# Optimization experiments

Measured on AMD Instinct MI355X. Metric: run time of the kernel, lower is better.

The kernel has to match this reference:

```python
import jax, jax.numpy as jnp
import numpy as np

# dims
B, T, NM, F = 2, 32512, 80, 128          # batch, samples, n_mels, frames
R, S, NC = 64, 128, 256                   # residual, skip, num_class channels
HOP, UK, KC = 256, 512, 2                 # hopsize, upsample kernel, causal kernel
MD, NCB = 10, 3                           # dilations per cycle (2^0..2^9), cycles
NB = MD * NCB                             # 30 residual blocks


def conv1d(x, w, b, dilation=1, pad=(0, 0), lhs_dilation=1):
    # x: [B,C,L], w: [O,I,K] (OIH), b: [O]
    y = jax.lax.conv_general_dilated(
        x, w, window_strides=(1,), padding=(pad,),
        lhs_dilation=(lhs_dilation,), rhs_dilation=(dilation,),
        dimension_numbers=('NCH', 'OIH', 'NCH'))
    return y + b[None, :, None]


def setup_inputs() -> dict:
    key = jax.random.key(0)
    ks = jax.random.split(key, 16)
    s = 0.05
    nrm = lambda k, shape: jax.random.normal(k, shape, dtype=jnp.float32) * s
    return {
        'x': jax.random.normal(ks[0], (B, T), dtype=jnp.float32),
        'mels': jax.random.normal(ks[1], (B, NM, F), dtype=jnp.float32),
        'input_w': nrm(ks[2], (R, 1, 1)), 'input_b': jnp.zeros((R,), jnp.float32),
        # mel upsampler (ConvTranspose1d), kernel stored in forward-conv OIH layout
        'mel_w': nrm(ks[3], (NM, NM, UK)), 'mel_b': jnp.zeros((NM,), jnp.float32),
        # 30 gated residual blocks, params stacked on leading axis
        'blk_dil_w': nrm(ks[4], (NB, 2 * R, R, KC)), 'blk_dil_b': jnp.zeros((NB, 2 * R), jnp.float32),
        'blk_cond_w': nrm(ks[5], (NB, 2 * R, NM, 1)), 'blk_cond_b': jnp.zeros((NB, 2 * R), jnp.float32),
        'blk_skip_w': nrm(ks[6], (NB, S, R, 1)), 'blk_skip_b': jnp.zeros((NB, S), jnp.float32),
        'blk_res_w': nrm(ks[7], (NB, R, R, 1)), 'blk_res_b': jnp.zeros((NB, R), jnp.float32),
        'post1_w': nrm(ks[8], (NC, S, 1)), 'post1_b': jnp.zeros((NC,), jnp.float32),
        'post2_w': nrm(ks[9], (NC, NC, 1)), 'post2_b': jnp.zeros((NC,), jnp.float32),
    }


def reference(x, mels, input_w, input_b, mel_w, mel_b,
              blk_dil_w, blk_dil_b, blk_cond_w, blk_cond_b,
              blk_skip_w, blk_skip_b, blk_res_w, blk_res_b,
              post1_w, post1_b, post2_w, post2_b):
    # ConvTranspose1d(stride=HOP, padding=UK//2) == lhs-dilated conv with pad UK-1-UK//2
    pt = UK - 1 - UK // 2
    cond = conv1d(mels, mel_w, mel_b, pad=(pt, pt), lhs_dilation=HOP)  # [B,NM,(F-1)*HOP]
    L = min(T, cond.shape[-1])
    cond = cond[..., :L]
    res = conv1d(x[:, None, :L], input_w, input_b)  # [B,R,L]
    skip = jnp.zeros((B, S, L), res.dtype)
    for i in range(NB):
        d = 2 ** (i % MD)
        z = (conv1d(res, blk_dil_w[i], blk_dil_b[i], dilation=d, pad=((KC - 1) * d, 0))
             + conv1d(cond, blk_cond_w[i], blk_cond_b[i]))  # [B,2R,L]
        f, g = jnp.split(z, 2, axis=1)
        h = jnp.tanh(f) * jax.nn.sigmoid(g)                 # gated activation
        skip = skip + conv1d(h, blk_skip_w[i], blk_skip_b[i])
        res = res + conv1d(h, blk_res_w[i], blk_res_b[i])
    y = conv1d(jax.nn.relu(skip), post1_w, post1_b)
    y = conv1d(jax.nn.relu(y), post2_w, post2_b)            # [B,NC,L]
    return y
```

## Files before the change

### kernel.cpp

```cpp
#include <hip/hip_runtime.h>
#include <math.h>

#define T_LEN 32512
#define NTILES 508
#define BATCH 2
#define NMEL 80
#define FRAMES 128
#define NBLK 30
#define NPAIRS 15
#define PAD 768
#define TP (T_LEN + PAD)

typedef short bfrag __attribute__((ext_vector_type(8)));
typedef float facc __attribute__((ext_vector_type(4)));
typedef ushort us4v __attribute__((ext_vector_type(4)));
typedef ushort us8v __attribute__((ext_vector_type(8)));

#define MFMA16(a, b, c) __builtin_amdgcn_mfma_f32_16x16x32_bf16((a), (b), (c), 0, 0, 0)

#define RESH_OFF   0u
#define CONDB_OFF  17039360u
#define WA_OFF     29818880u
#define WSF_OFF    31539200u
#define WRF_OFF    32030720u
#define WP1_OFF    32276480u
#define WP2_OFF    32342016u
#define ZB_OFF     32473088u
#define SBS_OFF    32488448u
#define SKIPG_OFF  32488960u
#define CONDA_OFF  SKIPG_OFF
#define HB_OFF     65781248u
#define SLOT_BYTES 8323072ull
#define SLOT_ELEMS 4161536ull
#define Y1R_OFF    82427392u
#undef Y1R_OFF
#define Y1R_OFF    165658112u

static __device__ __forceinline__ ushort f2bf(float f) {
  union { float f; unsigned int u; } v;
  v.f = f;
  unsigned int r = (v.u + 0x7FFFu + ((v.u >> 16) & 1u)) >> 16;
  return (ushort)r;
}
static __device__ __forceinline__ float bf2f(ushort h) {
  union { unsigned int u; float f; } v;
  v.u = ((unsigned int)h) << 16;
  return v.f;
}
static __device__ __forceinline__ float sigmoidf_(float x) {
  return 1.f / (1.f + __expf(-x));
}
static __device__ __forceinline__ float tanhf_(float x) {
  return 2.f / (1.f + __expf(-2.f * x)) - 1.f;
}
static __device__ __forceinline__ bfrag ldfrag(const ushort* p) {
  return *reinterpret_cast<const bfrag*>(p);
}
static __device__ __forceinline__ void gload_lds16(const void* g, void* l) {
  __builtin_amdgcn_global_load_lds(
      (const __attribute__((address_space(1))) unsigned int*)g,
      (__attribute__((address_space(3))) unsigned int*)l, 16, 0, 0);
}

__global__ __launch_bounds__(256) void prep_kernel(
    const float* __restrict__ dil_w, const float* __restrict__ cond_w,
    const float* __restrict__ skip_w, const float* __restrict__ res_w,
    const float* __restrict__ p1_w, const float* __restrict__ p2_w,
    const float* __restrict__ mel_w, const float* __restrict__ dil_b,
    const float* __restrict__ cond_b, const float* __restrict__ skip_b,
    ushort* __restrict__ wa, ushort* __restrict__ wsf, ushort* __restrict__ wrf,
    ushort* __restrict__ wp1, ushort* __restrict__ wp2,
    ushort* __restrict__ condA, float* __restrict__ zb,
    float* __restrict__ sbs) {
  int tid = blockIdx.x * blockDim.x + threadIdx.x;
  int stride = gridDim.x * blockDim.x;
  for (int idx = tid; idx < NBLK * 56 * 512; idx += stride) {
    int j = idx & 7, lane = (idx >> 3) & 63;
    int f = (idx >> 9) % 56, layer = idx / (56 * 512);
    int mt = f / 7, kt = f % 7;
    int m = 16 * mt + (lane & 15);
    int k = 32 * kt + 8 * (lane >> 4) + j;
    float v;
    if (k < 64)       v = dil_w[(((size_t)layer * 128 + m) * 64 + k) * 2 + 0];
    else if (k < 128) v = dil_w[(((size_t)layer * 128 + m) * 64 + (k - 64)) * 2 + 1];
    else if (k < 208) v = cond_w[((size_t)layer * 128 + m) * 80 + (k - 128)];
    else              v = 0.f;
    wa[idx] = f2bf(v);
  }
  for (int idx = tid; idx < NBLK * 16 * 512; idx += stride) {
    int j = idx & 7, lane = (idx >> 3) & 63;
    int f = (idx >> 9) & 15, layer = idx / (16 * 512);
    int mt = f >> 1, kt = f & 1;
    int m = 16 * mt + (lane & 15);
    int k = 32 * kt + 8 * (lane >> 4) + j;
    wsf[idx] = f2bf(skip_w[((size_t)layer * 128 + m) * 64 + k]);
  }
  for (int idx = tid; idx < NBLK * 8 * 512; idx += stride) {
    int j = idx & 7, lane = (idx >> 3) & 63;
    int f = (idx >> 9) & 7, layer = idx / (8 * 512);
    int mt = f >> 1, kt = f & 1;
    int m = 16 * mt + (lane & 15);
    int k = 32 * kt + 8 * (lane >> 4) + j;
    wrf[idx] = f2bf(res_w[((size_t)layer * 64 + m) * 64 + k]);
  }
  for (int idx = tid; idx < 64 * 512; idx += stride) {
    int j = idx & 7, lane = (idx >> 3) & 63;
    int f = idx >> 9;
    int mt = f >> 2, kt = f & 3;
    int m = 16 * mt + (lane & 15);
    int k = 32 * kt + 8 * (lane >> 4) + j;
    wp1[idx] = f2bf(p1_w[(size_t)m * 128 + k]);
  }
  for (int idx = tid; idx < 128 * 512; idx += stride) {
    int j = idx & 7, lane = (idx >> 3) & 63;
    int f = idx >> 9;
    int mt = f >> 3, kt = f & 7;
    int m = 16 * mt + (lane & 15);
    int k = 32 * kt + 8 * (lane >> 4) + j;
    wp2[idx] = f2bf(p2_w[(size_t)m * 256 + k]);
  }
  for (int idx = tid; idx < 25 * 512 * 256; idx += stride) {
    int q = idx & 511;
    int f = (idx >> 9) % 25;
    int u = idx / (25 * 512);
    int j = q & 7, lane = q >> 3;
    int mt = f / 5, kt = f % 5;
    int m = 16 * mt + (lane & 15);
    int k = 32 * kt + 8 * (lane >> 4) + j;
    int ci = (k < 80) ? k : k - 80;
    int kk = (k < 80) ? (255 - u) : (511 - u);
    condA[idx] = f2bf(mel_w[((size_t)m * 80 + ci) * 512 + kk]);
  }
  for (int idx = tid; idx < NBLK * 128; idx += stride)
    zb[idx] = dil_b[idx] + cond_b[idx];
  for (int idx = tid; idx < 128; idx += stride) {
    float s = 0.f;
    for (int i2 = 0; i2 < NBLK; ++i2) s += skip_b[i2 * 128 + idx];
    sbs[idx] = s;
  }
}

#define BSTR 168
__global__ __launch_bounds__(256) void cond_mfma(
    const float* __restrict__ mels, const ushort* __restrict__ condA,
    const float* __restrict__ mel_b, ushort* __restrict__ condb) {
  __shared__ ushort BT[128 * BSTR];
  const int tid = threadIdx.x;
  const int lane = tid & 63;
  const int w = tid >> 6;
  const int b = blockIdx.y;
  const int half = blockIdx.z;
  const int u = blockIdx.x * 4 + w;
  const int q4 = 4 * (lane >> 4);
  const int l15 = lane & 15;
  const float* melb = mels + (size_t)b * NMEL * FRAMES;
  for (int idx = tid; idx < 160 * 128; idx += 256) {
    int M = idx & 127;
    int k = idx >> 7;
    int ci = (k < 80) ? k : k - 80;
    int Mp = M + ((k < 80) ? 0 : 1);
    float v = (Mp < 128) ? melb[(size_t)ci * FRAMES + Mp] : 0.f;
    BT[M * BSTR + k] = f2bf(v);
  }
  __syncthreads();
  facc acc[5][4];
  #pragma unroll
  for (int mt = 0; mt < 5; ++mt) {
    #pragma unroll
    for (int nt = 0; nt < 4; ++nt) {
      #pragma unroll
      for (int r = 0; r < 4; ++r) acc[mt][nt][r] = mel_b[16 * mt + q4 + r];
    }
  }
  const ushort* cA = condA + (size_t)u * 25 * 512 + lane * 8;
  const int bofs = l15 * BSTR + 8 * (lane >> 4);
  #pragma unroll
  for (int kt = 0; kt < 5; ++kt) {
    bfrag a[5];
    #pragma unroll
    for (int mt = 0; mt < 5; ++mt) a[mt] = ldfrag(cA + (mt * 5 + kt) * 512);
    #pragma unroll
    for (int nt = 0; nt < 4; ++nt) {
      bfrag bb = ldfrag(&BT[(half * 64 + nt * 16) * BSTR + bofs + kt * 32]);
      #pragma unroll
      for (int mt = 0; mt < 5; ++mt) acc[mt][nt] = MFMA16(a[mt], bb, acc[mt][nt]);
    }
  }
  ushort* cbp = condb + (size_t)b * TP * 96;
  #pragma unroll
  for (int mt = 0; mt < 5; ++mt) {
    #pragma unroll
    for (int nt = 0; nt < 4; ++nt) {
      const int M = half * 64 + nt * 16 + l15;
      if (M < 127) {
        us4v p;
        #pragma unroll
        for (int r = 0; r < 4; ++r) p[r] = f2bf(acc[mt][nt][r]);
        const int t = M * 256 + u;
        *reinterpret_cast<us4v*>(&cbp[(size_t)(t + PAD) * 96 + 16 * mt + q4]) = p;
      }
    }
  }
}

__global__ __launch_bounds__(256) void init_res_kernel(
    const float* __restrict__ x, const float* __restrict__ iw,
    const float* __restrict__ ib, ushort* __restrict__ resh0) {
  int idx = blockIdx.x * blockDim.x + threadIdx.x;
  if (idx >= BATCH * T_LEN * 64) return;
  int c = idx & 63;
  int t = (idx >> 6) % T_LEN;
  int b = idx / (64 * T_LEN);
  float v = x[(size_t)b * T_LEN + t] * iw[c] + ib[c];
  resh0[(size_t)b * TP * 64 + (size_t)(t + PAD) * 64 + c] = f2bf(v);
}

template <int DEFER>
__global__ __launch_bounds__(256, 4) void wn_pair_kernel(
    const ushort* __restrict__ resh_in, ushort* __restrict__ resh_out,
    const ushort* __restrict__ condb, const ushort* __restrict__ wa,
    const ushort* __restrict__ wsf, const ushort* __restrict__ wrf,
    const float* __restrict__ zb, const float* __restrict__ res_b,
    const float* __restrict__ skip_b, float* __restrict__ skipg,
    ushort* __restrict__ hb0, ushort* __restrict__ hb1, int i0, int d0,
    int writeRes) {
  __shared__ ushort HT[64 * 72];
  __shared__ ushort RTs[64 * 72];
  __shared__ ushort RTh[64 * 72];
  const int i1 = i0 + 1;
  const int d1 = 2 * d0;
  const int tid = threadIdx.x;
  const int lane = tid & 63;
  const int w = tid >> 6;
  const int l15 = lane & 15;
  const int q4 = 4 * (lane >> 4);
  const int colq = 8 * (lane >> 4);
  const int orig = blockIdx.x;
  const int xcd = orig & 7;
  const int loc = orig >> 3;
  const int tile = (xcd < 4 ? xcd * 64 : 256 + (xcd - 4) * 63) + loc;
  const int t0 = tile * 64;
  const int t0s = t0 - d1;
  const int b = blockIdx.y;

  const ushort* rhi = resh_in + (size_t)b * TP * 64;
  ushort* rho = resh_out + (size_t)b * TP * 64;
  const ushort* cbp = condb + (size_t)b * TP * 96;
  const int bofs_h = l15 * 72 + colq;

  facc rs_s[4], rs_h[4], sk[8];
  facc accF[4], accG[4];
  if constexpr (!DEFER) {
    #pragma unroll
    for (int j = 0; j < 8; ++j) {
      const int ch = 32 * w + 16 * (j >> 2) + q4;
      facc s0 = *(const facc*)(skip_b + i0 * 128 + ch);
      facc s1 = *(const facc*)(skip_b + i1 * 128 + ch);
      sk[j] = s0 + s1;
    }
  }

#define ZG_INITB(LAYER)                                                       \
  _Pragma("unroll")                                                           \
  for (int nt = 0; nt < 4; ++nt) {                                            \
    accF[nt] = *(const facc*)(zb + (LAYER) * 128 + 16 * w + q4);              \
    accG[nt] = *(const facc*)(zb + (LAYER) * 128 + 64 + 16 * w + q4);         \
  }

#define ZG_GLOBAL(LAYER, TB)                                                  \
  {                                                                           \
    ZG_INITB(LAYER)                                                           \
    const ushort* wal = wa + (size_t)(LAYER) * 56 * 512 + lane * 8;           \
    const ushort* bp0[4];                                                     \
    const ushort* bp1[4];                                                     \
    const ushort* bpc[4];                                                     \
    _Pragma("unroll")                                                         \
    for (int nt = 0; nt < 4; ++nt) {                                          \
      const int tg = (TB) + nt * 16 + l15;                                    \
      bp0[nt] = rhi + (size_t)(tg - d0 + PAD) * 64 + colq;                    \
      bp1[nt] = rhi + (size_t)(tg + PAD) * 64 + colq;                         \
      bpc[nt] = cbp + (size_t)(tg + PAD) * 96 + colq;                         \
    }                                                                         \
    _Pragma("unroll")                                                         \
    for (int kt = 0; kt < 7; ++kt) {                                          \
      bfrag aF = ldfrag(wal + (w * 7 + kt) * 512);                            \
      bfrag aG = ldfrag(wal + ((w + 4) * 7 + kt) * 512);                      \
      _Pragma("unroll")                                                       \
      for (int nt = 0; nt < 4; ++nt) {                                        \
        bfrag bb = (kt < 2)   ? ldfrag(bp0[nt] + kt * 32)                     \
                   : (kt < 4) ? ldfrag(bp1[nt] + (kt - 2) * 32)               \
                              : ldfrag(bpc[nt] + (kt - 4) * 32);              \
        accF[nt] = MFMA16(aF, bb, accF[nt]);                                  \
        accG[nt] = MFMA16(aG, bb, accG[nt]);                                  \
      }                                                                       \
    }                                                                         \
  }

#define ZG_LDS(LAYER)                                                        \
  {                                                                           \
    ZG_INITB(LAYER)                                                           \
    const ushort* wal = wa + (size_t)(LAYER) * 56 * 512 + lane * 8;           \
    const ushort* bpc[4];                                                     \
    _Pragma("unroll")                                                         \
    for (int nt = 0; nt < 4; ++nt)                                            \
      bpc[nt] = cbp + (size_t)(t0 + nt * 16 + l15 + PAD) * 96 + colq;         \
    _Pragma("unroll")                                                         \
    for (int kt = 0; kt < 7; ++kt) {                                          \
      bfrag aF = ldfrag(wal + (w * 7 + kt) * 512);                            \
      bfrag aG = ldfrag(wal + ((w + 4) * 7 + kt) * 512);                      \
      _Pragma("unroll")                                                       \
      for (int nt = 0; nt < 4; ++nt) {                                        \
        bfrag bb = (kt < 2)                                                   \
            ? ldfrag(&RTs[(nt * 16 + l15) * 72 + kt * 32 + colq])             \
            : (kt < 4)                                                        \
                ? ldfrag(&RTh[(nt * 16 + l15) * 72 + (kt - 2) * 32 + colq])   \
                : ldfrag(bpc[nt] + (kt - 4) * 32);                            \
        accF[nt] = MFMA16(aF, bb, accF[nt]);                                  \
        accG[nt] = MFMA16(aG, bb, accG[nt]);                                  \
      }                                                                       \
    }                                                                         \
  }

#define GATE(HBPTR, DOHB)                                                     \
  {                                                                           \
    _Pragma("unroll")                                                         \
    for (int nt = 0; nt < 4; ++nt) {                                          \
      us4v p;                                                                 \
      _Pragma("unroll")                                                       \
      for (int r = 0; r < 4; ++r)                                             \
        p[r] = f2bf(tanhf_(accF[nt][r]) * sigmoidf_(accG[nt][r]));            \
      *reinterpret_cast<us4v*>(&HT[(nt * 16 + l15) * 72 + 16 * w + q4]) = p;  \
      if (DOHB)                                                               \
        *reinterpret_cast<us4v*>((HBPTR) + (size_t)b * T_LEN * 64 +           \
                                 (size_t)(t0 + nt * 16 + l15) * 64 +          \
                                 16 * w + q4) = p;                            \
    }                                                                         \
  }

#define RES_GEMM(LAYER, RS)                                                   \
  {                                                                           \
    const ushort* wrl = wrf + (size_t)(LAYER) * 8 * 512 + lane * 8;           \
    _Pragma("unroll")                                                         \
    for (int kt = 0; kt < 2; ++kt) {                                          \
      bfrag ar = ldfrag(wrl + (w * 2 + kt) * 512);                            \
      _Pragma("unroll")                                                       \
      for (int nt = 0; nt < 4; ++nt) {                                        \
        bfrag bb = ldfrag(&HT[nt * 16 * 72 + bofs_h + kt * 32]);              \
        RS[nt] = MFMA16(ar, bb, RS[nt]);                                      \
      }                                                                       \
    }                                                                         \
  }

#define SKIP_GEMM(LAYER)                                                      \
  {                                                                           \
    const ushort* wsl = wsf + (size_t)(LAYER) * 16 * 512 + lane * 8;          \
    _Pragma("unroll")                                                         \
    for (int kt = 0; kt < 2; ++kt) {                                          \
      bfrag a0 = ldfrag(wsl + ((2 * w) * 2 + kt) * 512);                      \
      bfrag a1 = ldfrag(wsl + ((2 * w + 1) * 2 + kt) * 512);                  \
      _Pragma("unroll")                                                       \
      for (int nt = 0; nt < 4; ++nt) {                                        \
        bfrag bb = ldfrag(&HT[nt * 16 * 72 + bofs_h + kt * 32]);              \
        sk[nt] = MFMA16(a0, bb, sk[nt]);                                      \
        sk[4 + nt] = MFMA16(a1, bb, sk[4 + nt]);                              \
      }                                                                       \
    }                                                                         \
  }

  ZG_GLOBAL(i0, t0s);
  GATE(hb0, 0);
  __syncthreads();
  #pragma unroll
  for (int nt = 0; nt < 4; ++nt) {
    const int tg = t0s + nt * 16 + l15;
    us4v hv = *(const us4v*)(rhi + (size_t)(tg + PAD) * 64 + 16 * w + q4);
    facc rbv = *(const facc*)(res_b + i0 * 64 + 16 * w + q4);
    #pragma unroll
    for (int r = 0; r < 4; ++r) rs_s[nt][r] = bf2f(hv[r]) + rbv[r];
  }
  RES_GEMM(i0, rs_s);
  #pragma unroll
  for (int nt = 0; nt < 4; ++nt) {
    const bool ok = (t0s + nt * 16 + l15) >= 0;
    us4v p;
    #pragma unroll
    for (int r = 0; r < 4; ++r) p[r] = ok ? f2bf(rs_s[nt][r]) : (ushort)0;
    *reinterpret_cast<us4v*>(&RTs[(nt * 16 + l15) * 72 + 16 * w + q4]) = p;
  }
  __syncthreads();
  ZG_GLOBAL(i0, t0);
  GATE(hb0, DEFER);
  __syncthreads();
  #pragma unroll
  for (int nt = 0; nt < 4; ++nt) {
    const int tg = t0 + nt * 16 + l15;
    us4v hv = *(const us4v*)(rhi + (size_t)(tg + PAD) * 64 + 16 * w + q4);
    facc rbv = *(const facc*)(res_b + i0 * 64 + 16 * w + q4);
    #pragma unroll
    for (int r = 0; r < 4; ++r) rs_h[nt][r] = bf2f(hv[r]) + rbv[r];
  }
  if constexpr (!DEFER) { SKIP_GEMM(i0); }
  RES_GEMM(i0, rs_h);
  #pragma unroll
  for (int nt = 0; nt < 4; ++nt) {
    us4v p;
    #pragma unroll
    for (int r = 0; r < 4; ++r) p[r] = f2bf(rs_h[nt][r]);
    *reinterpret_cast<us4v*>(&RTh[(nt * 16 + l15) * 72 + 16 * w + q4]) = p;
  }
  __syncthreads();
  ZG_LDS(i1);
  GATE(hb1, DEFER);
  __syncthreads();
  #pragma unroll
  for (int nt = 0; nt < 4; ++nt) {
    facc rbv = *(const facc*)(res_b + i1 * 64 + 16 * w + q4);
    rs_s[nt] = rs_h[nt] + rbv;
  }
  if constexpr (!DEFER) { SKIP_GEMM(i1); }
  RES_GEMM(i1, rs_s);
  if (writeRes) {
    #pragma unroll
    for (int nt = 0; nt < 4; ++nt) {
      const int tg = t0 + nt * 16 + l15;
      us4v p;
      #pragma unroll
      for (int r = 0; r < 4; ++r) p[r] = f2bf(rs_s[nt][r]);
      *reinterpret_cast<us4v*>(rho + (size_t)(tg + PAD) * 64 + 16 * w + q4) = p;
    }
  }
  if constexpr (!DEFER) {
    float* sg = skipg + (size_t)b * T_LEN * 128;
    #pragma unroll
    for (int nt = 0; nt < 4; ++nt) {
      const int tg = t0 + nt * 16 + l15;
      facc* p0 = (facc*)(sg + (size_t)tg * 128 + 32 * w + q4);
      facc* p1 = (facc*)(sg + (size_t)tg * 128 + 32 * w + 16 + q4);
      *p0 = *p0 + sk[nt];
      *p1 = *p1 + sk[4 + nt];
    }
  }
#undef ZG_INITB
#undef ZG_GLOBAL
#undef ZG_LDS
#undef GATE
#undef RES_GEMM
#undef SKIP_GEMM
}

template <int FIRST, int FUSE>
__global__ __launch_bounds__(256) void skip_accum(
    const ushort* __restrict__ hb, const ushort* __restrict__ wsf,
    float* __restrict__ skipg, const float* __restrict__ sbs,
    const ushort* __restrict__ wp1, const float* __restrict__ p1b,
    ushort* __restrict__ y1r, int base, int nl) {
  __shared__ ushort HL[12 * 2048];
  const int tid = threadIdx.x;
  const int lane = tid & 63;
  const int w = tid >> 6;
  const int l15 = lane & 15;
  const int q4 = 4 * (lane >> 4);
  const int colq = 8 * (lane >> 4);
  const int t0 = blockIdx.x * 32;
  const int b = blockIdx.y;

  {
    const int D = tid * 16;
    const int Dsw = D ^ (((D >> 7) & 7) << 4);
    const char* srcb =
        (const char*)(hb + (size_t)b * T_LEN * 64 + (size_t)t0 * 64);
    char* ldsb = (char*)HL + (tid >> 6) * 1024;
    for (int l = 0; l < nl; ++l)
      gload_lds16(srcb + (size_t)l * SLOT_BYTES + Dsw, ldsb + l * 4096);
  }

  float* sg = skipg + (size_t)b * T_LEN * 128;
  facc a0[2], a1[2];
  if constexpr (FIRST) {
    #pragma unroll
    for (int nt = 0; nt < 2; ++nt) {
      #pragma unroll
      for (int r = 0; r < 4; ++r) { a0[nt][r] = 0.f; a1[nt][r] = 0.f; }
    }
  } else {
    #pragma unroll
    for (int nt = 0; nt < 2; ++nt) {
      const int tg = t0 + nt * 16 + l15;
      a0[nt] = *(const facc*)(sg + (size_t)tg * 128 + 32 * w + q4);
      a1[nt] = *(const facc*)(sg + (size_t)tg * 128 + 32 * w + 16 + q4);
    }
  }
  __syncthreads();

  for (int l = 0; l < nl; ++l) {
    const ushort* wsl = wsf + (size_t)(base + l) * 16 * 512 + lane * 8;
    #pragma unroll
    for (int kt = 0; kt < 2; ++kt) {
      bfrag f0 = ldfrag(wsl + ((2 * w) * 2 + kt) * 512);
      bfrag f1 = ldfrag(wsl + ((2 * w + 1) * 2 + kt) * 512);
      #pragma unroll
      for (int nt = 0; nt < 2; ++nt) {
        const int t = nt * 16 + l15;
        int byteoff = t * 128 + kt * 64 + colq * 2;
        byteoff ^= ((t & 7) << 4);
        bfrag bb = ldfrag((const ushort*)((const char*)HL + l * 4096 + byteoff));
        a0[nt] = MFMA16(f0, bb, a0[nt]);
        a1[nt] = MFMA16(f1, bb, a1[nt]);
      }
    }
  }

  if constexpr (!FUSE) {
    #pragma unroll
    for (int nt = 0; nt < 2; ++nt) {
      const int tg = t0 + nt * 16 + l15;
      *(facc*)(sg + (size_t)tg * 128 + 32 * w + q4) = a0[nt];
      *(facc*)(sg + (size_t)tg * 128 + 32 * w + 16 + q4) = a1[nt];
    }
  } else {
    __syncthreads();
    ushort* ST = HL;
    #pragma unroll
    for (int nt = 0; nt < 2; ++nt) {
      us4v p0, p1;
      #pragma unroll
      for (int r = 0; r < 4; ++r) {
        p0[r] = f2bf(fmaxf(a0[nt][r] + sbs[32 * w + q4 + r], 0.f));
        p1[r] = f2bf(fmaxf(a1[nt][r] + sbs[32 * w + 16 + q4 + r], 0.f));
      }
      const int row = nt * 16 + l15;
      *reinterpret_cast<us4v*>(&ST[row * 136 + 32 * w + q4]) = p0;
      *reinterpret_cast<us4v*>(&ST[row * 136 + 32 * w + 16 + q4]) = p1;
    }
    __syncthreads();
    facc acc2[4][2];
    #pragma unroll
    for (int mi = 0; mi < 4; ++mi) {
      #pragma unroll
      for (int nt = 0; nt < 2; ++nt) {
        #pragma unroll
        for (int r = 0; r < 4; ++r)
          acc2[mi][nt][r] = p1b[16 * (4 * w + mi) + q4 + r];
      }
    }
    const int lo = lane * 8;
    #pragma unroll
    for (int kt = 0; kt < 4; ++kt) {
      bfrag am[4];
      #pragma unroll
      for (int mi = 0; mi < 4; ++mi)
        am[mi] = ldfrag(wp1 + ((4 * w + mi) * 4 + kt) * 512 + lo);
      #pragma unroll
      for (int nt = 0; nt < 2; ++nt) {
        bfrag bb = ldfrag(&ST[(nt * 16 + l15) * 136 + kt * 32 + colq]);
        #pragma unroll
        for (int mi = 0; mi < 4; ++mi)
          acc2[mi][nt] = MFMA16(am[mi], bb, acc2[mi][nt]);
      }
    }
    ushort* yb = y1r + (size_t)b * 256 * T_LEN;
    #pragma unroll
    for (int mi = 0; mi < 4; ++mi) {
      #pragma unroll
      for (int nt = 0; nt < 2; ++nt) {
        const int tt = t0 + nt * 16 + l15;
        #pragma unroll
        for (int r = 0; r < 4; ++r)
          yb[(size_t)(16 * (4 * w + mi) + q4 + r) * T_LEN + tt] =
              f2bf(fmaxf(acc2[mi][nt][r], 0.f));
      }
    }
  }
}

#define FSSTR 136
__global__ __launch_bounds__(256) void post1_mfma(
    const float* __restrict__ skipg, const float* __restrict__ sbs,
    const ushort* __restrict__ wp1, const float* __restrict__ p1b,
    ushort* __restrict__ y1r) {
  __shared__ ushort ST[64 * FSSTR];
  const int tid = threadIdx.x;
  const int lane = tid & 63;
  const int w = tid >> 6;
  const int t0 = blockIdx.x * 64;
  const int b = blockIdx.y;
  {
    const int t = tid & 63;
    const int kc = tid >> 6;
    const float* sp =
        skipg + (size_t)b * T_LEN * 128 + (size_t)(t0 + t) * 128 + kc * 32;
    #pragma unroll
    for (int j = 0; j < 8; ++j) {
      facc v = *(const facc*)(sp + j * 4);
      us4v o;
      #pragma unroll
      for (int r = 0; r < 4; ++r) {
        float s = sbs ? sbs[kc * 32 + j * 4 + r] : 0.f;
        o[r] = f2bf(fmaxf(v[r] + s, 0.f));
      }
      *reinterpret_cast<us4v*>(&ST[t * FSSTR + kc * 32 + j * 4]) = o;
    }
  }
  __syncthreads();
  const int q4 = 4 * (lane >> 4);
  facc acc[4][4];
  #pragma unroll
  for (int mi = 0; mi < 4; ++mi) {
    #pragma unroll
    for (int nt = 0; nt < 4; ++nt) {
      #pragma unroll
      for (int r = 0; r < 4; ++r)
        acc[mi][nt][r] = p1b[16 * (4 * w + mi) + q4 + r];
    }
  }
  const int lo = lane * 8;
  const int bofs = (lane & 15) * FSSTR + 8 * (lane >> 4);
  #pragma unroll
  for (int kt = 0; kt < 4; ++kt) {
    bfrag a[4];
    #pragma unroll
    for (int mi = 0; mi < 4; ++mi)
      a[mi] = ldfrag(wp1 + ((4 * w + mi) * 4 + kt) * 512 + lo);
    #pragma unroll
    for (int nt = 0; nt < 4; ++nt) {
      bfrag bb = ldfrag(&ST[nt * 16 * FSSTR + bofs + kt * 32]);
      #pragma unroll
      for (int mi = 0; mi < 4; ++mi) acc[mi][nt] = MFMA16(a[mi], bb, acc[mi][nt]);
    }
  }
  ushort* yb = y1r + (size_t)b * 256 * T_LEN;
  #pragma unroll
  for (int mi = 0; mi < 4; ++mi) {
    #pragma unroll
    for (int nt = 0; nt < 4; ++nt) {
      const int tt = t0 + nt * 16 + (lane & 15);
      #pragma unroll
      for (int r = 0; r < 4; ++r)
        yb[(size_t)(16 * (4 * w + mi) + q4 + r) * T_LEN + tt] =
            f2bf(fmaxf(acc[mi][nt][r], 0.f));
    }
  }
}

#define YSTR 264
__global__ __launch_bounds__(256) void post2_mfma(
    const ushort* __restrict__ y1r, const ushort* __restrict__ wp2,
    const float* __restrict__ p2b, float* __restrict__ out) {
  __shared__ ushort YT[64 * YSTR];
  const int tid = threadIdx.x;
  const int lane = tid & 63;
  const int w = tid >> 6;
  const int t0 = blockIdx.x * 64;
  const int b = blockIdx.y;
  const ushort* yb = y1r + (size_t)b * 256 * T_LEN;
  const int t = t0 + lane;
  for (int kc = 0; kc < 8; ++kc) {
    int k0 = w * 64 + kc * 8;
    us8v v;
    #pragma unroll
    for (int j = 0; j < 8; ++j) v[j] = yb[(size_t)(k0 + j) * T_LEN + t];
    *reinterpret_cast<us8v*>(&YT[lane * YSTR + k0]) = v;
  }
  __syncthreads();
  const int q4 = 4 * (lane >> 4);
  facc acc[4][4];
  #pragma unroll
  for (int mi = 0; mi < 4; ++mi) {
    #pragma unroll
    for (int nt = 0; nt < 4; ++nt) {
      #pragma unroll
      for (int r = 0; r < 4; ++r)
        acc[mi][nt][r] = p2b[16 * (4 * w + mi) + q4 + r];
    }
  }
  const int lo = lane * 8;
  const int bofs = (lane & 15) * YSTR + 8 * (lane >> 4);
  #pragma unroll
  for (int kt = 0; kt < 8; ++kt) {
    bfrag a[4];
    #pragma unroll
    for (int mi = 0; mi < 4; ++mi)
      a[mi] = ldfrag(wp2 + ((4 * w + mi) * 8 + kt) * 512 + lo);
    #pragma unroll
    for (int nt = 0; nt < 4; ++nt) {
      bfrag bb = ldfrag(&YT[nt * 16 * YSTR + bofs + kt * 32]);
      #pragma unroll
      for (int mi = 0; mi < 4; ++mi) acc[mi][nt] = MFMA16(a[mi], bb, acc[mi][nt]);
    }
  }
  float* ob = out + (size_t)b * 256 * T_LEN;
  #pragma unroll
  for (int mi = 0; mi < 4; ++mi) {
    #pragma unroll
    for (int nt = 0; nt < 4; ++nt) {
      const int tt = t0 + nt * 16 + (lane & 15);
      #pragma unroll
      for (int r = 0; r < 4; ++r)
        ob[(size_t)(16 * (4 * w + mi) + q4 + r) * T_LEN + tt] = acc[mi][nt][r];
    }
  }
}

extern "C" void kernel_launch(void* const* d_in, const int* in_sizes, int n_in,
                              void* d_out, int out_size, void* d_ws,
                              size_t ws_size, hipStream_t stream) {
  const float* x       = (const float*)d_in[0];
  const float* mels    = (const float*)d_in[1];
  const float* input_w = (const float*)d_in[2];
  const float* input_b = (const float*)d_in[3];
  const float* mel_w   = (const float*)d_in[4];
  const float* mel_b   = (const float*)d_in[5];
  const float* dil_w   = (const float*)d_in[6];
  const float* dil_b   = (const float*)d_in[7];
  const float* cond_w  = (const float*)d_in[8];
  const float* cond_b  = (const float*)d_in[9];
  const float* skip_w  = (const float*)d_in[10];
  const float* skip_b  = (const float*)d_in[11];
  const float* res_w   = (const float*)d_in[12];
  const float* res_b   = (const float*)d_in[13];
  const float* p1_w    = (const float*)d_in[14];
  const float* p1_b    = (const float*)d_in[15];
  const float* p2_w    = (const float*)d_in[16];
  const float* p2_b    = (const float*)d_in[17];

  char* ws = (char*)d_ws;
  ushort* rhA   = (ushort*)(ws + RESH_OFF);
  ushort* rhB   = rhA + (size_t)2 * TP * 64;
  ushort* condb = (ushort*)(ws + CONDB_OFF);
  ushort* wa    = (ushort*)(ws + WA_OFF);
  ushort* wsf   = (ushort*)(ws + WSF_OFF);
  ushort* wrf   = (ushort*)(ws + WRF_OFF);
  ushort* wp1   = (ushort*)(ws + WP1_OFF);
  ushort* wp2   = (ushort*)(ws + WP2_OFF);
  float* zbp    = (float*)(ws + ZB_OFF);
  float* sbsp   = (float*)(ws + SBS_OFF);
  float* skipg  = (float*)(ws + SKIPG_OFF);
  ushort* condA = (ushort*)(ws + CONDA_OFF);
  ushort* hbuf  = (ushort*)(ws + HB_OFF);
  ushort* y1rp  = (ushort*)(ws + Y1R_OFF);
  float* out    = (float*)d_out;

  int G = 0;
  if (ws_size >= (size_t)Y1R_OFF + 33292288ull) {
    G = 6;
  } else if (ws_size >= (size_t)HB_OFF + 2ull * SLOT_BYTES + 33292288ull) {
    G = (int)((ws_size - HB_OFF - 33292288ull) / (2ull * SLOT_BYTES));
    if (G > 6) G = 6;
    y1rp = (ushort*)(ws + HB_OFF + (size_t)(2 * G) * SLOT_BYTES);
  }
  const bool defer = (G >= 1);

  for (int k = 0; k < 2; ++k)
    for (int b = 0; b < 2; ++b)
      hipMemsetAsync((char*)(k == 0 ? rhA : rhB) + (size_t)b * TP * 64 * 2, 0,
                     (size_t)PAD * 64 * 2, stream);
  hipMemsetAsync(condb, 0, (size_t)2 * TP * 96 * 2, stream);

  prep_kernel<<<2048, 256, 0, stream>>>(dil_w, cond_w, skip_w, res_w, p1_w,
                                        p2_w, mel_w, dil_b, cond_b, skip_b, wa,
                                        wsf, wrf, wp1, wp2, condA, zbp, sbsp);
  cond_mfma<<<dim3(64, BATCH, 2), 256, 0, stream>>>(mels, condA, mel_b, condb);
  if (!defer) {
    hipMemsetAsync(skipg, 0, (size_t)2 * T_LEN * 128 * 4, stream);
  }
  init_res_kernel<<<(BATCH * T_LEN * 64 + 255) / 256, 256, 0, stream>>>(
      x, input_w, input_b, rhA);

  ushort* rhi = rhA;
  ushort* rho = rhB;
  int groupStart = 0;
  const dim3 ag(T_LEN / 32, BATCH);
  for (int p = 0; p < NPAIRS; ++p) {
    int i0 = 2 * p;
    int d0 = 1 << (i0 % 10);
    int wr = (p < NPAIRS - 1) ? 1 : 0;
    if (defer) {
      ushort* h0 = hbuf + (size_t)(2 * (p - groupStart)) * SLOT_ELEMS;
      wn_pair_kernel<1><<<dim3(NTILES, BATCH), 256, 0, stream>>>(
          rhi, rho, condb, wa, wsf, wrf, zbp, res_b, skip_b, skipg, h0,
          h0 + SLOT_ELEMS, i0, d0, wr);
      if (p - groupStart + 1 == G || p == NPAIRS - 1) {
        int nl = 2 * (p - groupStart + 1);
        int base = 2 * groupStart;
        bool isF = (groupStart == 0);
        bool isL = (p == NPAIRS - 1);
        if (isF && isL)
          skip_accum<1, 1><<<ag, 256, 0, stream>>>(hbuf, wsf, skipg, sbsp, wp1,
                                                   p1_b, y1rp, base, nl);
        else if (isF)
          skip_accum<1, 0><<<ag, 256, 0, stream>>>(hbuf, wsf, skipg, sbsp, wp1,
                                                   p1_b, y1rp, base, nl);
        else if (isL)
          skip_accum<0, 1><<<ag, 256, 0, stream>>>(hbuf, wsf, skipg, sbsp, wp1,
                                                   p1_b, y1rp, base, nl);
        else
          skip_accum<0, 0><<<ag, 256, 0, stream>>>(hbuf, wsf, skipg, sbsp, wp1,
                                                   p1_b, y1rp, base, nl);
        groupStart = p + 1;
      }
    } else {
      wn_pair_kernel<0><<<dim3(NTILES, BATCH), 256, 0, stream>>>(
          rhi, rho, condb, wa, wsf, wrf, zbp, res_b, skip_b, skipg, nullptr,
          nullptr, i0, d0, wr);
    }
    ushort* th = rhi; rhi = rho; rho = th;
  }

  if (!defer) {
    post1_mfma<<<dim3(NTILES, BATCH), 256, 0, stream>>>(skipg, nullptr, wp1,
                                                        p1_b, y1rp);
  }
  post2_mfma<<<dim3(NTILES, BATCH), 256, 0, stream>>>(y1rp, wp2, p2_b, out);
}
```

Before: 848.5 us.

## Stage residual and cond tiles into swizzled LDS via async global-to-LDS loads

```diff
diff --git a/kernel.cpp b/kernel.cpp
--- a/kernel.cpp
+++ b/kernel.cpp
@@ -32,8 +32,6 @@
 #define HB_OFF     65781248u
 #define SLOT_BYTES 8323072ull
 #define SLOT_ELEMS 4161536ull
-#define Y1R_OFF    82427392u
-#undef Y1R_OFF
 #define Y1R_OFF    165658112u
 
 static __device__ __forceinline__ ushort f2bf(float f) {
@@ -216,7 +214,7 @@
 }
 
 template <int DEFER>
-__global__ __launch_bounds__(256, 4) void wn_pair_kernel(
+__global__ __launch_bounds__(256, 3) void wn_pair_kernel(
     const ushort* __restrict__ resh_in, ushort* __restrict__ resh_out,
     const ushort* __restrict__ condb, const ushort* __restrict__ wa,
     const ushort* __restrict__ wsf, const ushort* __restrict__ wrf,
@@ -224,17 +222,17 @@
     const float* __restrict__ skip_b, float* __restrict__ skipg,
     ushort* __restrict__ hb0, ushort* __restrict__ hb1, int i0, int d0,
     int writeRes) {
-  __shared__ ushort HT[64 * 72];
-  __shared__ ushort RTs[64 * 72];
-  __shared__ ushort RTh[64 * 72];
+  __shared__ char XT1[16384];
+  __shared__ char XT2[16384];
+  __shared__ char CT[16384];
   const int i1 = i0 + 1;
   const int d1 = 2 * d0;
   const int tid = threadIdx.x;
   const int lane = tid & 63;
   const int w = tid >> 6;
   const int l15 = lane & 15;
-  const int q4 = 4 * (lane >> 4);
-  const int colq = 8 * (lane >> 4);
+  const int g = lane >> 4;
+  const int q4 = 4 * g;
   const int orig = blockIdx.x;
   const int xcd = orig & 7;
   const int loc = orig >> 3;
@@ -246,19 +244,40 @@
   const ushort* rhi = resh_in + (size_t)b * TP * 64;
   ushort* rho = resh_out + (size_t)b * TP * 64;
   const ushort* cbp = condb + (size_t)b * TP * 96;
-  const int bofs_h = l15 * 72 + colq;
-
-  facc rs_s[4], rs_h[4], sk[8];
-  facc accF[4], accG[4];
+
+  #pragma unroll
+  for (int j = 0; j < 4; ++j) {
+    const int D = w * 4096 + j * 1024 + lane * 16;
+    const int Ls = D ^ (((D >> 8) & 7) << 4);
+    const int row = Ls >> 8;
+    const int half = (Ls >> 7) & 1;
+    const int off = Ls & 127;
+    const char* s1 = (const char*)(rhi +
+        (size_t)(t0s + row - (half ? 0 : d0) + PAD) * 64) + off;
+    gload_lds16(s1, XT1 + D);
+    const char* s2 = (const char*)(rhi +
+        (size_t)(t0 + row - (half ? 0 : d0) + PAD) * 64) + off;
+    gload_lds16(s2, XT2 + D);
+    const int offc = Ls & 255;
+    const char* s3 = (offc < 192)
+        ? (const char*)cbp + (size_t)(t0 + row + PAD) * 192 + offc
+        : (const char*)cbp + offc;
+    gload_lds16(s3, CT + D);
+  }
+
+  facc accF[4], accG[4], rs_s[4], rs_h[4], sk[8];
   if constexpr (!DEFER) {
     #pragma unroll
-    for (int j = 0; j < 8; ++j) {
-      const int ch = 32 * w + 16 * (j >> 2) + q4;
+    for (int jj = 0; jj < 8; ++jj) {
+      const int ch = 32 * w + 16 * (jj >> 2) + q4;
       facc s0 = *(const facc*)(skip_b + i0 * 128 + ch);
       facc s1 = *(const facc*)(skip_b + i1 * 128 + ch);
-      sk[j] = s0 + s1;
-    }
-  }
+      sk[jj] = s0 + s1;
+    }
+  }
+
+#define LDSF(BUF, r, x) \
+  ldfrag((const ushort*)((BUF) + ((((r) * 256 + (x)) ^ (((r) & 7) << 4)))))
 
 #define ZG_INITB(LAYER)                                                       \
   _Pragma("unroll")                                                           \
@@ -267,61 +286,70 @@
     accG[nt] = *(const facc*)(zb + (LAYER) * 128 + 64 + 16 * w + q4);         \
   }
 
-#define ZG_GLOBAL(LAYER, TB)                                                  \
+#define ZG_S(LAYER)                                                           \
   {                                                                           \
     ZG_INITB(LAYER)                                                           \
     const ushort* wal = wa + (size_t)(LAYER) * 56 * 512 + lane * 8;           \
-    const ushort* bp0[4];                                                     \
-    const ushort* bp1[4];                                                     \
     const ushort* bpc[4];                                                     \
     _Pragma("unroll")                                                         \
-    for (int nt = 0; nt < 4; ++nt) {                                          \
-      const int tg = (TB) + nt * 16 + l15;                                    \
-      bp0[nt] = rhi + (size_t)(tg - d0 + PAD) * 64 + colq;                    \
-      bp1[nt] = rhi + (size_t)(tg + PAD) * 64 + colq;                         \
-      bpc[nt] = cbp + (size_t)(tg + PAD) * 96 + colq;                         \
-    }                                                                         \
+    for (int nt = 0; nt < 4; ++nt)                                            \
+      bpc[nt] = cbp + (size_t)(t0s + nt * 16 + l15 + PAD) * 96 + 8 * g;       \
     _Pragma("unroll")                                                         \
     for (int kt = 0; kt < 7; ++kt) {                                          \
       bfrag aF = ldfrag(wal + (w * 7 + kt) * 512);                            \
       bfrag aG = ldfrag(wal + ((w + 4) * 7 + kt) * 512);                      \
       _Pragma("unroll")                                                       \
       for (int nt = 0; nt < 4; ++nt) {                                        \
-        bfrag bb = (kt < 2)   ? ldfrag(bp0[nt] + kt * 32)                     \
-                   : (kt < 4) ? ldfrag(bp1[nt] + (kt - 2) * 32)               \
-                              : ldfrag(bpc[nt] + (kt - 4) * 32);              \
+        const int r = nt * 16 + l15;                                          \
+        bfrag bb = (kt < 4) ? LDSF(XT1, r, kt * 64 + 16 * g)                  \
+                            : ldfrag(bpc[nt] + (kt - 4) * 32);                \
         accF[nt] = MFMA16(aF, bb, accF[nt]);                                  \
         accG[nt] = MFMA16(aG, bb, accG[nt]);                                  \
       }                                                                       \
     }                                                                         \
   }
 
-#define ZG_LDS(LAYER)                                                        \
+#define ZG_H(LAYER)                                                           \
   {                                                                           \
     ZG_INITB(LAYER)                                                           \
     const ushort* wal = wa + (size_t)(LAYER) * 56 * 512 + lane * 8;           \
-    const ushort* bpc[4];                                                     \
-    _Pragma("unroll")                                                         \
-    for (int nt = 0; nt < 4; ++nt)                                            \
-      bpc[nt] = cbp + (size_t)(t0 + nt * 16 + l15 + PAD) * 96 + colq;         \
     _Pragma("unroll")                                                         \
     for (int kt = 0; kt < 7; ++kt) {                                          \
       bfrag aF = ldfrag(wal + (w * 7 + kt) * 512);                            \
       bfrag aG = ldfrag(wal + ((w + 4) * 7 + kt) * 512);                      \
       _Pragma("unroll")                                                       \
       for (int nt = 0; nt < 4; ++nt) {                                        \
-        bfrag bb = (kt < 2)                                                   \
-            ? ldfrag(&RTs[(nt * 16 + l15) * 72 + kt * 32 + colq])             \
-            : (kt < 4)                                                        \
-                ? ldfrag(&RTh[(nt * 16 + l15) * 72 + (kt - 2) * 32 + colq])   \
-                : ldfrag(bpc[nt] + (kt - 4) * 32);                            \
+        const int r = nt * 16 + l15;                                          \
+        bfrag bb = (kt < 4) ? LDSF(XT2, r, kt * 64 + 16 * g)                  \
+                            : LDSF(CT, r, (kt - 4) * 64 + 16 * g);            \
         accF[nt] = MFMA16(aF, bb, accF[nt]);                                  \
         accG[nt] = MFMA16(aG, bb, accG[nt]);                                  \
       }                                                                       \
     }                                                                         \
   }
 
-#define GATE(HBPTR, DOHB)                                                     \
+#define ZG_I1(LAYER)                                                          \
+  {                                                                           \
+    ZG_INITB(LAYER)                                                           \
+    const ushort* wal = wa + (size_t)(LAYER) * 56 * 512 + lane * 8;           \
+    _Pragma("unroll")                                                         \
+    for (int kt = 0; kt < 7; ++kt) {                                          \
+      bfrag aF = ldfrag(wal + (w * 7 + kt) * 512);                            \
+      bfrag aG = ldfrag(wal + ((w + 4) * 7 + kt) * 512);                      \
+      _Pragma("unroll")                                                       \
+      for (int nt = 0; nt < 4; ++nt) {                                        \
+        const int r = nt * 16 + l15;                                          \
+        bfrag bb = (kt < 2)                                                   \
+            ? LDSF(XT1, r, 128 + kt * 64 + 16 * g)                            \
+            : (kt < 4) ? LDSF(XT2, r, 128 + (kt - 2) * 64 + 16 * g)           \
+                       : LDSF(CT, r, (kt - 4) * 64 + 16 * g);                 \
+        accF[nt] = MFMA16(aF, bb, accF[nt]);                                  \
+        accG[nt] = MFMA16(aG, bb, accG[nt]);                                  \
+      }                                                                       \
+    }                                                                         \
+  }
+
+#define GATE(BUF, HBPTR, DOHB)                                                \
   {                                                                           \
     _Pragma("unroll")                                                         \
     for (int nt = 0; nt < 4; ++nt) {                                          \
@@ -329,15 +357,16 @@
       _Pragma("unroll")                                                       \
       for (int r = 0; r < 4; ++r)                                             \
         p[r] = f2bf(tanhf_(accF[nt][r]) * sigmoidf_(accG[nt][r]));            \
-      *reinterpret_cast<us4v*>(&HT[(nt * 16 + l15) * 72 + 16 * w + q4]) = p;  \
+      const int row = nt * 16 + l15;                                          \
+      const int byo = (row * 256 + 32 * w + 8 * g) ^ ((row & 7) << 4);        \
+      *reinterpret_cast<us4v*>((BUF) + byo) = p;                              \
       if (DOHB)                                                               \
         *reinterpret_cast<us4v*>((HBPTR) + (size_t)b * T_LEN * 64 +           \
-                                 (size_t)(t0 + nt * 16 + l15) * 64 +          \
-                                 16 * w + q4) = p;                            \
+                                 (size_t)(t0 + row) * 64 + 16 * w + q4) = p;  \
     }                                                                         \
   }
 
-#define RES_GEMM(LAYER, RS)                                                   \
+#define RES_GEMM(LAYER, HTBUF, RS)                                            \
   {                                                                           \
     const ushort* wrl = wrf + (size_t)(LAYER) * 8 * 512 + lane * 8;           \
     _Pragma("unroll")                                                         \
@@ -345,13 +374,14 @@
       bfrag ar = ldfrag(wrl + (w * 2 + kt) * 512);                            \
       _Pragma("unroll")                                                       \
       for (int nt = 0; nt < 4; ++nt) {                                        \
-        bfrag bb = ldfrag(&HT[nt * 16 * 72 + bofs_h + kt * 32]);              \
+        const int r = nt * 16 + l15;                                          \
+        bfrag bb = LDSF(HTBUF, r, kt * 64 + 16 * g);                          \
         RS[nt] = MFMA16(ar, bb, RS[nt]);                                      \
       }                                                                       \
     }                                                                         \
   }
 
-#define SKIP_GEMM(LAYER)                                                      \
+#define SKIP_GEMM(LAYER, HTBUF)                                               \
   {                                                                           \
     const ushort* wsl = wsf + (size_t)(LAYER) * 16 * 512 + lane * 8;          \
     _Pragma("unroll")                                                         \
@@ -360,16 +390,33 @@
       bfrag a1 = ldfrag(wsl + ((2 * w + 1) * 2 + kt) * 512);                  \
       _Pragma("unroll")                                                       \
       for (int nt = 0; nt < 4; ++nt) {                                        \
-        bfrag bb = ldfrag(&HT[nt * 16 * 72 + bofs_h + kt * 32]);              \
+        const int r = nt * 16 + l15;                                          \
+        bfrag bb = LDSF(HTBUF, r, kt * 64 + 16 * g);                          \
         sk[nt] = MFMA16(a0, bb, sk[nt]);                                      \
         sk[4 + nt] = MFMA16(a1, bb, sk[4 + nt]);                              \
       }                                                                       \
     }                                                                         \
   }
 
-  ZG_GLOBAL(i0, t0s);
-  GATE(hb0, 0);
-  __syncthreads();
+#define RT_WRITE(BUF, RS, GUARD)                                              \
+  {                                                                           \
+    _Pragma("unroll")                                                         \
+    for (int nt = 0; nt < 4; ++nt) {                                          \
+      us4v p;                                                                 \
+      const bool ok = !(GUARD) || (t0s + nt * 16 + l15) >= 0;                 \
+      _Pragma("unroll")                                                       \
+      for (int r = 0; r < 4; ++r) p[r] = ok ? f2bf(RS[nt][r]) : (ushort)0;    \
+      const int row = nt * 16 + l15;                                          \
+      const int byo = (row * 256 + 128 + 32 * w + 8 * g) ^ ((row & 7) << 4);  \
+      *reinterpret_cast<us4v*>((BUF) + byo) = p;                              \
+    }                                                                         \
+  }
+
+  __syncthreads();
+
+  ZG_S(i0);
+  __syncthreads();
+  GATE(XT1, hb0, 0);
   #pragma unroll
   for (int nt = 0; nt < 4; ++nt) {
     const int tg = t0s + nt * 16 + l15;
@@ -378,19 +425,12 @@
     #pragma unroll
     for (int r = 0; r < 4; ++r) rs_s[nt][r] = bf2f(hv[r]) + rbv[r];
   }
-  RES_GEMM(i0, rs_s);
-  #pragma unroll
-  for (int nt = 0; nt < 4; ++nt) {
-    const bool ok = (t0s + nt * 16 + l15) >= 0;
-    us4v p;
-    #pragma unroll
-    for (int r = 0; r < 4; ++r) p[r] = ok ? f2bf(rs_s[nt][r]) : (ushort)0;
-    *reinterpret_cast<us4v*>(&RTs[(nt * 16 + l15) * 72 + 16 * w + q4]) = p;
-  }
-  __syncthreads();
-  ZG_GLOBAL(i0, t0);
-  GATE(hb0, DEFER);
-  __syncthreads();
+  __syncthreads();
+  RES_GEMM(i0, XT1, rs_s);
+  RT_WRITE(XT1, rs_s, 1);
+  ZG_H(i0);
+  __syncthreads();
+  GATE(XT2, hb0, DEFER);
   #pragma unroll
   for (int nt = 0; nt < 4; ++nt) {
     const int tg = t0 + nt * 16 + l15;
@@ -399,26 +439,21 @@
     #pragma unroll
     for (int r = 0; r < 4; ++r) rs_h[nt][r] = bf2f(hv[r]) + rbv[r];
   }
-  if constexpr (!DEFER) { SKIP_GEMM(i0); }
-  RES_GEMM(i0, rs_h);
-  #pragma unroll
-  for (int nt = 0; nt < 4; ++nt) {
-    us4v p;
-    #pragma unroll
-    for (int r = 0; r < 4; ++r) p[r] = f2bf(rs_h[nt][r]);
-    *reinterpret_cast<us4v*>(&RTh[(nt * 16 + l15) * 72 + 16 * w + q4]) = p;
-  }
-  __syncthreads();
-  ZG_LDS(i1);
-  GATE(hb1, DEFER);
-  __syncthreads();
+  __syncthreads();
+  if constexpr (!DEFER) { SKIP_GEMM(i0, XT2); }
+  RES_GEMM(i0, XT2, rs_h);
+  RT_WRITE(XT2, rs_h, 0);
+  __syncthreads();
+  ZG_I1(i1);
+  GATE(XT1, hb1, DEFER);
   #pragma unroll
   for (int nt = 0; nt < 4; ++nt) {
     facc rbv = *(const facc*)(res_b + i1 * 64 + 16 * w + q4);
     rs_s[nt] = rs_h[nt] + rbv;
   }
-  if constexpr (!DEFER) { SKIP_GEMM(i1); }
-  RES_GEMM(i1, rs_s);
+  __syncthreads();
+  if constexpr (!DEFER) { SKIP_GEMM(i1, XT1); }
+  RES_GEMM(i1, XT1, rs_s);
   if (writeRes) {
     #pragma unroll
     for (int nt = 0; nt < 4; ++nt) {
@@ -440,12 +475,15 @@
       *p1 = *p1 + sk[4 + nt];
     }
   }
+#undef LDSF
 #undef ZG_INITB
-#undef ZG_GLOBAL
-#undef ZG_LDS
+#undef ZG_S
+#undef ZG_H
+#undef ZG_I1
 #undef GATE
 #undef RES_GEMM
 #undef SKIP_GEMM
+#undef RT_WRITE
 }
 
 template <int FIRST, int FUSE>
```

After: 697.8 us. 1.22x faster.
